# Kernel optimization log

Measured on AMD Instinct MI355X. Metric: run time of the kernel, lower is better.

The kernel has to match this reference:

```python
import jax, jax.numpy as jnp
import numpy as np

N = 100000      # nodes
E = 1_600_000   # edges
IN = 128        # in_channels
HID = 32        # hidden_channels (per head)
HEADS = 4
NC = 10         # num_classes
NEG_SLOPE = 0.2 # GATConv leaky relu slope
BN_EPS = 1e-5


def _gat_conv(x, src, dst, W, a_src, a_dst, bias, heads, out_ch, concat):
    # x: [N, F_in]; W: [F_in, heads*out_ch]; a_src/a_dst: [heads, out_ch]
    n = x.shape[0]
    h = (x @ W).reshape(n, heads, out_ch)                    # [N,H,C]
    al_src = jnp.sum(h * a_src, axis=-1)                     # [N,H]
    al_dst = jnp.sum(h * a_dst, axis=-1)                     # [N,H]
    e = jax.nn.leaky_relu(al_src[src] + al_dst[dst], NEG_SLOPE)  # [E,H]
    # segment softmax over destination node
    m = jax.ops.segment_max(e, dst, num_segments=n)          # [N,H]
    ex = jnp.exp(e - m[dst])
    s = jax.ops.segment_sum(ex, dst, num_segments=n)         # [N,H]
    alpha = ex / (s[dst] + 1e-16)                            # [E,H]
    out = jax.ops.segment_sum(h[src] * alpha[:, :, None], dst, num_segments=n)  # [N,H,C]
    if concat:
        out = out.reshape(n, heads * out_ch)
    else:
        out = out.mean(axis=1)
    return out + bias


def _bn(x, gamma, beta, mean, var):
    # eval-mode BatchNorm1d with running stats
    return (x - mean) * jax.lax.rsqrt(var + BN_EPS) * gamma + beta


def setup_inputs() -> dict:
    key = jax.random.key(0)
    ks = iter(jax.random.split(key, 40))
    d = {}
    d['x'] = jax.random.normal(next(ks), (N, IN), dtype=jnp.float32)
    d['edge_index'] = jax.random.randint(next(ks), (2, E), 0, N, dtype=jnp.int32)
    dims = [(IN, HID, HEADS), (HID * HEADS, HID, HEADS), (HID * HEADS, HID, 1)]
    for i, (fin, c, h) in enumerate(dims):
        d[f'W{i}'] = jax.random.normal(next(ks), (fin, h * c), dtype=jnp.float32) * (1.0 / np.sqrt(fin))
        d[f'as{i}'] = jax.random.normal(next(ks), (h, c), dtype=jnp.float32) * 0.1
        d[f'ad{i}'] = jax.random.normal(next(ks), (h, c), dtype=jnp.float32) * 0.1
        bdim = h * c if i < 2 else c
        d[f'b{i}'] = jnp.zeros((bdim,), dtype=jnp.float32)
        d[f'g{i}'] = jax.random.uniform(next(ks), (bdim,), dtype=jnp.float32, minval=0.5, maxval=1.5)
        d[f'bt{i}'] = jax.random.normal(next(ks), (bdim,), dtype=jnp.float32) * 0.1
        d[f'm{i}'] = jax.random.normal(next(ks), (bdim,), dtype=jnp.float32) * 0.1
        d[f'v{i}'] = jax.random.uniform(next(ks), (bdim,), dtype=jnp.float32, minval=0.5, maxval=1.5)
    d['Wc'] = jax.random.normal(next(ks), (HID, NC), dtype=jnp.float32) * (1.0 / np.sqrt(HID))
    d['bc'] = jnp.zeros((NC,), dtype=jnp.float32)
    return d


def reference(x, edge_index, W0, as0, ad0, b0, g0, bt0, m0, v0,
              W1, as1, ad1, b1, g1, bt1, m1, v1,
              W2, as2, ad2, b2, g2, bt2, m2, v2, Wc, bc):
    src, dst = edge_index[0], edge_index[1]
    # layer 0: concat heads
    h = _gat_conv(x, src, dst, W0, as0, ad0, b0, HEADS, HID, True)
    h = jax.nn.elu(_bn(h, g0, bt0, m0, v0))
    # layer 1: concat heads
    h = _gat_conv(h, src, dst, W1, as1, ad1, b1, HEADS, HID, True)
    h = jax.nn.elu(_bn(h, g1, bt1, m1, v1))
    # layer 2: single head, no concat
    h = _gat_conv(h, src, dst, W2, as2, ad2, b2, 1, HID, False)
    h = jax.nn.elu(_bn(h, g2, bt2, m2, v2))
    # dropout is identity in eval mode
    return h @ Wc + bc
```

## Files before the change

### kernel.cpp

```cpp
#include <hip/hip_runtime.h>
#include <hip/hip_bf16.h>
#include <math.h>

#define NN   100000
#define NE   1600000
#define FIN  128
#define HID  32
#define NHEADS 4
#define NCLS 10

typedef unsigned int uint32;
typedef __fp16 half2_t __attribute__((ext_vector_type(2)));
typedef __fp16 half8_t __attribute__((ext_vector_type(8)));
typedef float  f32x4   __attribute__((ext_vector_type(4)));

__device__ __forceinline__ uint32 packh2(float a, float b) {
    half2_t h = __builtin_amdgcn_cvt_pkrtz(a, b);
    return __builtin_bit_cast(uint32, h);
}
__device__ __forceinline__ float h_lo(uint32 v) {
    return (float)__builtin_bit_cast(half2_t, v)[0];
}
__device__ __forceinline__ float h_hi(uint32 v) {
    return (float)__builtin_bit_cast(half2_t, v)[1];
}
__device__ __forceinline__ half8_t as_h8(uint4 v) {
    return __builtin_bit_cast(half8_t, v);
}

__global__ void zero_i32(int* __restrict__ p, int n) {
    int i = blockIdx.x * blockDim.x + threadIdx.x;
    if (i < n) p[i] = 0;
}

__global__ void hist_rank_kernel(const int* __restrict__ dst, int* __restrict__ cnt,
                                 int* __restrict__ rank, int e) {
    const int t0 = blockIdx.x * (blockDim.x * 4) + threadIdx.x;
    int d[4];
    bool a[4];
#pragma unroll
    for (int k = 0; k < 4; ++k) {
        const int j = t0 + k * 256;
        a[k] = (j < e);
        d[k] = a[k] ? dst[j] : 0;
    }
    int r[4];
#pragma unroll
    for (int k = 0; k < 4; ++k)
        if (a[k]) r[k] = atomicAdd(&cnt[d[k]], 1);
#pragma unroll
    for (int k = 0; k < 4; ++k) {
        const int j = t0 + k * 256;
        if (a[k]) rank[j] = r[k];
    }
}

__global__ void scan_block_sums(const int* __restrict__ cnt, int* __restrict__ bsum, int n) {
    __shared__ int sm[256];
    int i = blockIdx.x * 256 + threadIdx.x;
    int v = (i < n) ? cnt[i] : 0;
    sm[threadIdx.x] = v;
    __syncthreads();
    for (int off = 128; off > 0; off >>= 1) {
        if (threadIdx.x < off) sm[threadIdx.x] += sm[threadIdx.x + off];
        __syncthreads();
    }
    if (threadIdx.x == 0) bsum[blockIdx.x] = sm[0];
}

__global__ void scan_single(const int* __restrict__ bsum, int* __restrict__ boff, int nb) {
    __shared__ int sm[512];
    int t = threadIdx.x;
    int v = (t < nb) ? bsum[t] : 0;
    sm[t] = v;
    __syncthreads();
    for (int off = 1; off < 512; off <<= 1) {
        int u = (t >= off) ? sm[t - off] : 0;
        __syncthreads();
        sm[t] += u;
        __syncthreads();
    }
    if (t < nb) boff[t] = sm[t] - v;
}

__global__ void scan_final(const int* __restrict__ cnt, const int* __restrict__ boff,
                           int* __restrict__ rowptr, int n) {
    __shared__ int sm[256];
    int i = blockIdx.x * 256 + threadIdx.x;
    int v = (i < n) ? cnt[i] : 0;
    sm[threadIdx.x] = v;
    __syncthreads();
    for (int off = 1; off < 256; off <<= 1) {
        int u = (threadIdx.x >= off) ? sm[threadIdx.x - off] : 0;
        __syncthreads();
        sm[threadIdx.x] += u;
        __syncthreads();
    }
    int incl = sm[threadIdx.x];
    int excl = incl - v;
    if (i < n) rowptr[i] = boff[blockIdx.x] + excl;
    if (i == n - 1) rowptr[n] = boff[blockIdx.x] + incl;
}

__global__ void scatter_kernel(const int* __restrict__ src, const int* __restrict__ dst,
                               const int* __restrict__ rank, const int* __restrict__ rowptr,
                               int* __restrict__ esrc, int e) {
    const int t0 = blockIdx.x * (blockDim.x * 4) + threadIdx.x;
#pragma unroll
    for (int k = 0; k < 4; ++k) {
        const int j = t0 + k * 256;
        if (j < e) {
            const int d = dst[j];
            esrc[rowptr[d] + rank[j]] = src[j];
        }
    }
}

__global__ void conv_x_kernel(const float* __restrict__ x, uint32* __restrict__ Xh, int n4) {
    int i = blockIdx.x * blockDim.x + threadIdx.x;
    if (i >= n4) return;
    const float4 v = ((const float4*)x)[i];
    ((uint2*)Xh)[i] = make_uint2(packh2(v.x, v.y), packh2(v.z, v.w));
}

__global__ void conv_w_kernel(const float* __restrict__ W0, const float* __restrict__ W1,
                              const float* __restrict__ W2, uint32* __restrict__ Wt0,
                              uint32* __restrict__ Wt1, uint32* __restrict__ Wt2) {
    int t = blockIdx.x * blockDim.x + threadIdx.x;
    if (t < 8192) {
        const int nn = t >> 6, ku = t & 63;
        Wt0[t] = packh2(W0[(2 * ku) * 128 + nn], W0[(2 * ku + 1) * 128 + nn]);
    } else if (t < 16384) {
        const int l = t - 8192;
        const int nn = l >> 6, ku = l & 63;
        Wt1[l] = packh2(W1[(2 * ku) * 128 + nn], W1[(2 * ku + 1) * 128 + nn]);
    } else if (t < 18432) {
        const int l = t - 16384;
        const int nn = l >> 6, ku = l & 63;
        Wt2[l] = packh2(W2[(2 * ku) * 32 + nn], W2[(2 * ku + 1) * 32 + nn]);
    }
}

template <int FOUT, int H>
__global__ __launch_bounds__(256) void gemm_mfma(const uint32* __restrict__ Xh,
                                                 const uint32* __restrict__ Wt,
                                                 const float* __restrict__ a_s,
                                                 const float* __restrict__ a_d,
                                                 float* __restrict__ alS,
                                                 float* __restrict__ alD,
                                                 uint32* __restrict__ Outh, int n) {
    constexpr int NT = FOUT / 16;
    const int wave = threadIdx.x >> 6;
    const int lane = threadIdx.x & 63;
    const int c = lane & 15;
    const int q = lane >> 4;
    const int row0 = blockIdx.x * 128 + wave * 32;

    int r0 = row0 + c;
    int r1 = row0 + 16 + c;
    if (r0 >= n) r0 = n - 1;
    if (r1 >= n) r1 = n - 1;

    f32x4 acc[2][NT];
#pragma unroll
    for (int m = 0; m < 2; ++m)
#pragma unroll
        for (int nt = 0; nt < NT; ++nt) acc[m][nt] = (f32x4){0.f, 0.f, 0.f, 0.f};

    const uint4* XU = (const uint4*)Xh;
    const uint4* WU = (const uint4*)Wt;

#pragma unroll
    for (int ks = 0; ks < 4; ++ks) {
        const half8_t a0 = as_h8(XU[(size_t)r0 * 16 + ks * 4 + q]);
        const half8_t a1 = as_h8(XU[(size_t)r1 * 16 + ks * 4 + q]);
#pragma unroll
        for (int nt = 0; nt < NT; ++nt) {
            const half8_t b = as_h8(WU[(nt * 16 + c) * 16 + ks * 4 + q]);
            acc[0][nt] = __builtin_amdgcn_mfma_f32_16x16x32_f16(a0, b, acc[0][nt], 0, 0, 0);
            acc[1][nt] = __builtin_amdgcn_mfma_f32_16x16x32_f16(a1, b, acc[1][nt], 0, 0, 0);
        }
    }

    float asv[NT], adv[NT];
#pragma unroll
    for (int nt = 0; nt < NT; ++nt) {
        asv[nt] = a_s[c + 16 * nt];
        adv[nt] = a_d[c + 16 * nt];
    }

#pragma unroll
    for (int m = 0; m < 2; ++m) {
#pragma unroll
        for (int reg = 0; reg < 4; ++reg) {
            const int grow = row0 + m * 16 + q * 4 + reg;
            const bool ok = (grow < n);
            if constexpr (H == 4) {
                float ps[4], pd[4];
#pragma unroll
                for (int h = 0; h < 4; ++h) {
                    ps[h] = acc[m][2 * h][reg] * asv[2 * h] + acc[m][2 * h + 1][reg] * asv[2 * h + 1];
                    pd[h] = acc[m][2 * h][reg] * adv[2 * h] + acc[m][2 * h + 1][reg] * adv[2 * h + 1];
                }
#pragma unroll
                for (int off = 1; off < 16; off <<= 1) {
#pragma unroll
                    for (int h = 0; h < 4; ++h) {
                        ps[h] += __shfl_xor(ps[h], off);
                        pd[h] += __shfl_xor(pd[h], off);
                    }
                }
                if (c < 4 && ok) {
                    const float vs = (c == 0) ? ps[0] : (c == 1) ? ps[1] : (c == 2) ? ps[2] : ps[3];
                    const float vd = (c == 0) ? pd[0] : (c == 1) ? pd[1] : (c == 2) ? pd[2] : pd[3];
                    alS[(size_t)grow * 4 + c] = vs;
                    alD[(size_t)grow * 4 + c] = vd;
                }
            } else {
                float ps = acc[m][0][reg] * asv[0] + acc[m][1][reg] * asv[1];
                float pd = acc[m][0][reg] * adv[0] + acc[m][1][reg] * adv[1];
#pragma unroll
                for (int off = 1; off < 16; off <<= 1) {
                    ps += __shfl_xor(ps, off);
                    pd += __shfl_xor(pd, off);
                }
                if (c == 0 && ok) {
                    alS[grow] = ps;
                    alD[grow] = pd;
                }
            }
#pragma unroll
            for (int nt = 0; nt < NT; ++nt) {
                const float v = acc[m][nt][reg];
                const float o = __shfl_xor(v, 1);
                if (((c & 1) == 0) && ok) {
                    Outh[(size_t)grow * (FOUT / 2) + nt * 8 + (c >> 1)] = packh2(v, o);
                }
            }
        }
    }
}

template <int H, int C>
__global__ __launch_bounds__(256) void gat_aggregate(
    const uint32* __restrict__ Hb,
    const int* __restrict__ rowptr, const int* __restrict__ esrc,
    const float* __restrict__ alS, const float* __restrict__ alD,
    const float* __restrict__ bias, const float* __restrict__ gamma,
    const float* __restrict__ beta, const float* __restrict__ bnmean,
    const float* __restrict__ bnvar, uint32* __restrict__ B16, int n) {
    constexpr int F  = H * C;
    constexpr int RW = F / 2;
    constexpr int NW = 4;
    __shared__ __align__(16) int   s_src[NW][68];
    __shared__ __align__(16) float s_ex[NW][H][68];

    const int wave = threadIdx.x >> 6;
    const int lane = threadIdx.x & 63;
    const int d    = blockIdx.x * NW + wave;
    if (d >= n) return;

    if (lane < 4) {
        s_src[wave][64 + lane] = 0;
#pragma unroll
        for (int h = 0; h < H; ++h) s_ex[wave][h][64 + lane] = 0.f;
    }
    __builtin_amdgcn_wave_barrier();

    const int beg = rowptr[d], end = rowptr[d + 1];
    float al_d[H], sl[H];
#pragma unroll
    for (int h = 0; h < H; ++h) {
        al_d[h] = alD[(size_t)d * H + h];
        sl[h]   = 0.f;
    }
    float acc0 = 0.f, acc1 = 0.f;
    const int head = (H == 4) ? (lane >> 4) : 0;

    for (int base = beg; base < end; base += 64) {
        const int j   = base + lane;
        const bool act = (j < end);
        int sj = 0;
        float ex[H];
        if (act) {
            sj = esrc[j];
            if constexpr (H == 4) {
                float4 av = *(const float4*)(alS + (size_t)sj * 4);
                float t0 = av.x + al_d[0], t1 = av.y + al_d[1];
                float t2 = av.z + al_d[2], t3 = av.w + al_d[3];
                t0 = t0 > 0.f ? t0 : 0.2f * t0;
                t1 = t1 > 0.f ? t1 : 0.2f * t1;
                t2 = t2 > 0.f ? t2 : 0.2f * t2;
                t3 = t3 > 0.f ? t3 : 0.2f * t3;
                ex[0] = __expf(t0); ex[1] = __expf(t1);
                ex[2] = __expf(t2); ex[3] = __expf(t3);
            } else {
                float t0 = alS[sj] + al_d[0];
                t0 = t0 > 0.f ? t0 : 0.2f * t0;
                ex[0] = __expf(t0);
            }
        } else {
#pragma unroll
            for (int h = 0; h < H; ++h) ex[h] = 0.f;
        }
#pragma unroll
        for (int h = 0; h < H; ++h) {
            s_ex[wave][h][lane] = ex[h];
            sl[h] += ex[h];
        }
        s_src[wave][lane] = sj;
        __builtin_amdgcn_wave_barrier();

        const int cc = min(64, end - base);
        if constexpr (H == 4) {
            const int ccr = (cc + 7) & ~7;
            for (int jj = 0; jj < ccr; jj += 8) {
                const int4   sa = *(const int4*)  &s_src[wave][jj];
                const int4   sb = *(const int4*)  &s_src[wave][jj + 4];
                const float4 wa = *(const float4*)&s_ex[wave][head][jj];
                const float4 wb = *(const float4*)&s_ex[wave][head][jj + 4];
                const int b0 = __builtin_amdgcn_readfirstlane(sa.x);
                const int b1 = __builtin_amdgcn_readfirstlane(sa.y);
                const int b2 = __builtin_amdgcn_readfirstlane(sa.z);
                const int b3 = __builtin_amdgcn_readfirstlane(sa.w);
                const int b4 = __builtin_amdgcn_readfirstlane(sb.x);
                const int b5 = __builtin_amdgcn_readfirstlane(sb.y);
                const int b6 = __builtin_amdgcn_readfirstlane(sb.z);
                const int b7 = __builtin_amdgcn_readfirstlane(sb.w);
                const uint32 v0 = Hb[(size_t)b0 * RW + lane];
                const uint32 v1 = Hb[(size_t)b1 * RW + lane];
                const uint32 v2 = Hb[(size_t)b2 * RW + lane];
                const uint32 v3 = Hb[(size_t)b3 * RW + lane];
                const uint32 v4 = Hb[(size_t)b4 * RW + lane];
                const uint32 v5 = Hb[(size_t)b5 * RW + lane];
                const uint32 v6 = Hb[(size_t)b6 * RW + lane];
                const uint32 v7 = Hb[(size_t)b7 * RW + lane];
                acc0 = fmaf(h_lo(v0), wa.x, acc0); acc1 = fmaf(h_hi(v0), wa.x, acc1);
                acc0 = fmaf(h_lo(v1), wa.y, acc0); acc1 = fmaf(h_hi(v1), wa.y, acc1);
                acc0 = fmaf(h_lo(v2), wa.z, acc0); acc1 = fmaf(h_hi(v2), wa.z, acc1);
                acc0 = fmaf(h_lo(v3), wa.w, acc0); acc1 = fmaf(h_hi(v3), wa.w, acc1);
                acc0 = fmaf(h_lo(v4), wb.x, acc0); acc1 = fmaf(h_hi(v4), wb.x, acc1);
                acc0 = fmaf(h_lo(v5), wb.y, acc0); acc1 = fmaf(h_hi(v5), wb.y, acc1);
                acc0 = fmaf(h_lo(v6), wb.z, acc0); acc1 = fmaf(h_hi(v6), wb.z, acc1);
                acc0 = fmaf(h_lo(v7), wb.w, acc0); acc1 = fmaf(h_hi(v7), wb.w, acc1);
            }
        } else {
            const int g  = lane >> 4;
            const int li = lane & 15;
            for (int jj = 0; jj < cc; jj += 4) {
                const int   idx = jj + g;
                const int   sj2 = s_src[wave][idx];
                const float w   = s_ex[wave][0][idx];
                const uint32 v  = Hb[(size_t)sj2 * RW + li];
                acc0 = fmaf(h_lo(v), w, acc0);
                acc1 = fmaf(h_hi(v), w, acc1);
            }
        }
        __builtin_amdgcn_wave_barrier();
    }

#pragma unroll
    for (int h = 0; h < H; ++h) {
#pragma unroll
        for (int off = 32; off > 0; off >>= 1) sl[h] += __shfl_xor(sl[h], off);
    }
    float sh;
    if constexpr (H == 4) {
        float a = (head & 1) ? sl[1] : sl[0];
        float b = (head & 1) ? sl[3] : sl[2];
        sh = (head & 2) ? b : a;
    } else {
        sh = sl[0];
        acc0 += __shfl_xor(acc0, 16); acc0 += __shfl_xor(acc0, 32);
        acc1 += __shfl_xor(acc1, 16); acc1 += __shfl_xor(acc1, 32);
    }

    const float inv = 1.f / (sh + 1e-16f);
    const int li  = (F == 128) ? lane : (lane & 15);
    const int c0 = 2 * li, c1 = 2 * li + 1;
    const bool wr = (F == 128) || (lane < 16);
    if (wr) {
        float o0 = acc0 * inv, o1 = acc1 * inv;
        float y0 = (o0 + bias[c0] - bnmean[c0]) * rsqrtf(bnvar[c0] + 1e-5f) * gamma[c0] + beta[c0];
        float y1 = (o1 + bias[c1] - bnmean[c1]) * rsqrtf(bnvar[c1] + 1e-5f) * gamma[c1] + beta[c1];
        y0 = y0 > 0.f ? y0 : expm1f(y0);
        y1 = y1 > 0.f ? y1 : expm1f(y1);
        B16[(size_t)d * RW + li] = packh2(y0, y1);
    }
}

__global__ void classifier_kernel(const uint32* __restrict__ H3, const float* __restrict__ Wc,
                                  const float* __restrict__ bc, float* __restrict__ out, int n) {
    int t  = blockIdx.x * blockDim.x + threadIdx.x;
    int ni = t / NCLS, c = t % NCLS;
    if (ni >= n) return;
    const uint32* row = H3 + (size_t)ni * 16;
    float a = bc[c];
#pragma unroll
    for (int u = 0; u < 16; ++u) {
        const uint32 v = row[u];
        a = fmaf(h_lo(v), Wc[(2 * u) * NCLS + c], a);
        a = fmaf(h_hi(v), Wc[(2 * u + 1) * NCLS + c], a);
    }
    out[(size_t)ni * NCLS + c] = a;
}

static inline char* align256(char* p) {
    return (char*)(((uintptr_t)p + 255) & ~(uintptr_t)255);
}

extern "C" void kernel_launch(void* const* d_in, const int* in_sizes, int n_in,
                              void* d_out, int out_size, void* d_ws, size_t ws_size,
                              hipStream_t stream) {
    const float* x  = (const float*)d_in[0];
    const int*   ei = (const int*)d_in[1];
    const int N = in_sizes[0] / FIN;
    const int E = in_sizes[1] / 2;
    const int* src = ei;
    const int* dst = ei + E;

    const float *W0 = (const float*)d_in[2],  *as0 = (const float*)d_in[3],
                *ad0 = (const float*)d_in[4], *b0 = (const float*)d_in[5],
                *g0 = (const float*)d_in[6],  *bt0 = (const float*)d_in[7],
                *m0 = (const float*)d_in[8],  *v0 = (const float*)d_in[9];
    const float *W1 = (const float*)d_in[10], *as1 = (const float*)d_in[11],
                *ad1 = (const float*)d_in[12],*b1 = (const float*)d_in[13],
                *g1 = (const float*)d_in[14], *bt1 = (const float*)d_in[15],
                *m1 = (const float*)d_in[16], *v1 = (const float*)d_in[17];
    const float *W2 = (const float*)d_in[18], *as2 = (const float*)d_in[19],
                *ad2 = (const float*)d_in[20],*b2 = (const float*)d_in[21],
                *g2 = (const float*)d_in[22], *bt2 = (const float*)d_in[23],
                *m2 = (const float*)d_in[24], *v2 = (const float*)d_in[25];
    const float *Wc = (const float*)d_in[26], *bc = (const float*)d_in[27];
    float* out = (float*)d_out;

    char* p = (char*)d_ws;
    uint32* Xh  = (uint32*)p;   p = align256(p + (size_t)N * 64 * 4);
    uint32* Ht  = (uint32*)p;   p = align256(p + (size_t)N * 64 * 4);
    uint32* B16 = (uint32*)p;   p = align256(p + (size_t)N * 64 * 4);
    uint32* Wt0 = (uint32*)p;   p = align256(p + 8192 * 4);
    uint32* Wt1 = (uint32*)p;   p = align256(p + 8192 * 4);
    uint32* Wt2 = (uint32*)p;   p = align256(p + 2048 * 4);
    float* alS = (float*)p;     p = align256(p + (size_t)N * NHEADS * 4);
    float* alD = (float*)p;     p = align256(p + (size_t)N * NHEADS * 4);
    int* cnt = (int*)p;         p = align256(p + (size_t)N * 4);
    int* rowptr = (int*)p;      p = align256(p + (size_t)(N + 1) * 4);
    int* rank = (int*)p;        p = align256(p + (size_t)E * 4);
    int* esrc = (int*)p;        p = align256(p + (size_t)E * 4);
    int* bsum = (int*)p;        p = align256(p + 512 * 4);
    int* boff = (int*)p;        p = align256(p + 512 * 4);
    (void)ws_size; (void)n_in; (void)out_size;

    const int NB = (N + 255) / 256;
    const int EB4 = (E + 1023) / 1024;

    zero_i32<<<NB, 256, 0, stream>>>(cnt, N);
    hist_rank_kernel<<<EB4, 256, 0, stream>>>(dst, cnt, rank, E);
    scan_block_sums<<<NB, 256, 0, stream>>>(cnt, bsum, N);
    scan_single<<<1, 512, 0, stream>>>(bsum, boff, NB);
    scan_final<<<NB, 256, 0, stream>>>(cnt, boff, rowptr, N);
    scatter_kernel<<<EB4, 256, 0, stream>>>(src, dst, rank, rowptr, esrc, E);

    conv_x_kernel<<<(N * 32 + 255) / 256, 256, 0, stream>>>(x, Xh, N * 32);
    conv_w_kernel<<<72, 256, 0, stream>>>(W0, W1, W2, Wt0, Wt1, Wt2);

    const int GB = (N + 127) / 128;
    const int AB = (N + 3) / 4;

    gemm_mfma<128, 4><<<GB, 256, 0, stream>>>(Xh, Wt0, as0, ad0, alS, alD, Ht, N);
    gat_aggregate<4, 32><<<AB, 256, 0, stream>>>(Ht, rowptr, esrc, alS, alD,
                                                 b0, g0, bt0, m0, v0, B16, N);
    gemm_mfma<128, 4><<<GB, 256, 0, stream>>>(B16, Wt1, as1, ad1, alS, alD, Ht, N);
    gat_aggregate<4, 32><<<AB, 256, 0, stream>>>(Ht, rowptr, esrc, alS, alD,
                                                 b1, g1, bt1, m1, v1, B16, N);
    gemm_mfma<32, 1><<<GB, 256, 0, stream>>>(B16, Wt2, as2, ad2, alS, alD, Ht, N);
    gat_aggregate<1, 32><<<AB, 256, 0, stream>>>(Ht, rowptr, esrc, alS, alD,
                                                 b2, g2, bt2, m2, v2, B16, N);
    classifier_kernel<<<(N * NCLS + 255) / 256, 256, 0, stream>>>(B16, Wc, bc, out, N);
}
```

Measured before the change: 546.0 us.

## Restructure GAT aggregation to per-lane uint4 gathers and fold BN constants

Measured after the change: 545.3 us. About the same (-0.1%).

```diff
diff --git a/kernel.cpp b/kernel.cpp
--- a/kernel.cpp
+++ b/kernel.cpp
@@ -141,6 +141,26 @@
     }
 }
 
+__global__ void bn_prep_kernel(
+    const float* __restrict__ b0, const float* __restrict__ g0, const float* __restrict__ bt0,
+    const float* __restrict__ m0, const float* __restrict__ v0,
+    const float* __restrict__ b1, const float* __restrict__ g1, const float* __restrict__ bt1,
+    const float* __restrict__ m1, const float* __restrict__ v1,
+    const float* __restrict__ b2, const float* __restrict__ g2, const float* __restrict__ bt2,
+    const float* __restrict__ m2, const float* __restrict__ v2,
+    float* __restrict__ A, float* __restrict__ B) {
+    const int t = threadIdx.x;
+    const float *b, *g, *bt, *m, *v;
+    int c;
+    if (t < 128)      { b = b0; g = g0; bt = bt0; m = m0; v = v0; c = t; }
+    else if (t < 256) { b = b1; g = g1; bt = bt1; m = m1; v = v1; c = t - 128; }
+    else if (t < 288) { b = b2; g = g2; bt = bt2; m = m2; v = v2; c = t - 256; }
+    else return;
+    const float s = g[c] * rsqrtf(v[c] + 1e-5f);
+    A[t] = s;
+    B[t] = bt[c] + (b[c] - m[c]) * s;
+}
+
 template <int FOUT, int H>
 __global__ __launch_bounds__(256) void gemm_mfma(const uint32* __restrict__ Xh,
                                                  const uint32* __restrict__ Wt,
@@ -246,146 +266,87 @@
     const uint32* __restrict__ Hb,
     const int* __restrict__ rowptr, const int* __restrict__ esrc,
     const float* __restrict__ alS, const float* __restrict__ alD,
-    const float* __restrict__ bias, const float* __restrict__ gamma,
-    const float* __restrict__ beta, const float* __restrict__ bnmean,
-    const float* __restrict__ bnvar, uint32* __restrict__ B16, int n) {
-    constexpr int F  = H * C;
-    constexpr int RW = F / 2;
-    constexpr int NW = 4;
-    __shared__ __align__(16) int   s_src[NW][68];
-    __shared__ __align__(16) float s_ex[NW][H][68];
+    const float* __restrict__ bnA, const float* __restrict__ bnB,
+    uint32* __restrict__ B16, int n) {
+    constexpr int F    = H * C;
+    constexpr int RU4  = F / 8;
+    constexpr int SLOTS = 64 / RU4;
+    constexpr int UNROLL = 16 / SLOTS;
 
     const int wave = threadIdx.x >> 6;
     const int lane = threadIdx.x & 63;
-    const int d    = blockIdx.x * NW + wave;
+    int d = blockIdx.x * 4 + wave;
     if (d >= n) return;
-
-    if (lane < 4) {
-        s_src[wave][64 + lane] = 0;
-#pragma unroll
-        for (int h = 0; h < H; ++h) s_ex[wave][h][64 + lane] = 0.f;
-    }
-    __builtin_amdgcn_wave_barrier();
-
-    const int beg = rowptr[d], end = rowptr[d + 1];
-    float al_d[H], sl[H];
-#pragma unroll
-    for (int h = 0; h < H; ++h) {
-        al_d[h] = alD[(size_t)d * H + h];
-        sl[h]   = 0.f;
-    }
-    float acc0 = 0.f, acc1 = 0.f;
-    const int head = (H == 4) ? (lane >> 4) : 0;
-
-    for (int base = beg; base < end; base += 64) {
-        const int j   = base + lane;
-        const bool act = (j < end);
-        int sj = 0;
-        float ex[H];
-        if (act) {
-            sj = esrc[j];
-            if constexpr (H == 4) {
-                float4 av = *(const float4*)(alS + (size_t)sj * 4);
-                float t0 = av.x + al_d[0], t1 = av.y + al_d[1];
-                float t2 = av.z + al_d[2], t3 = av.w + al_d[3];
-                t0 = t0 > 0.f ? t0 : 0.2f * t0;
-                t1 = t1 > 0.f ? t1 : 0.2f * t1;
-                t2 = t2 > 0.f ? t2 : 0.2f * t2;
-                t3 = t3 > 0.f ? t3 : 0.2f * t3;
-                ex[0] = __expf(t0); ex[1] = __expf(t1);
-                ex[2] = __expf(t2); ex[3] = __expf(t3);
-            } else {
-                float t0 = alS[sj] + al_d[0];
-                t0 = t0 > 0.f ? t0 : 0.2f * t0;
-                ex[0] = __expf(t0);
-            }
-        } else {
-#pragma unroll
-            for (int h = 0; h < H; ++h) ex[h] = 0.f;
+    d = __builtin_amdgcn_readfirstlane(d);
+
+    const int li = lane & (RU4 - 1);
+    const int g  = lane / RU4;
+    const int head = (H == 4) ? (li >> 2) : 0;
+
+    const float ald = alD[(size_t)d * H + head];
+    const int beg = rowptr[d];
+    const int end = rowptr[d + 1];
+    const int endm1 = end - 1;
+
+    float acc[8];
+#pragma unroll
+    for (int k = 0; k < 8; ++k) acc[k] = 0.f;
+    float den = 0.f;
+
+    const uint4* HbU4 = (const uint4*)Hb;
+
+    for (int base = beg; base < end; base += 16) {
+#pragma unroll
+        for (int u = 0; u < UNROLL; ++u) {
+            const int j  = base + u * SLOTS + g;
+            const bool act = (j < end);
+            const int jc = act ? j : endm1;
+            const int sj = esrc[jc];
+            const float aw = (H == 4) ? alS[(size_t)sj * 4 + head] : alS[sj];
+            float t = aw + ald;
+            t = fmaxf(t, 0.2f * t);
+            const float ex = act ? __expf(t) : 0.f;
+            den += ex;
+            const uint4 v = HbU4[(size_t)sj * RU4 + li];
+            acc[0] = fmaf(h_lo(v.x), ex, acc[0]);
+            acc[1] = fmaf(h_hi(v.x), ex, acc[1]);
+            acc[2] = fmaf(h_lo(v.y), ex, acc[2]);
+            acc[3] = fmaf(h_hi(v.y), ex, acc[3]);
+            acc[4] = fmaf(h_lo(v.z), ex, acc[4]);
+            acc[5] = fmaf(h_hi(v.z), ex, acc[5]);
+            acc[6] = fmaf(h_lo(v.w), ex, acc[6]);
+            acc[7] = fmaf(h_hi(v.w), ex, acc[7]);
         }
-#pragma unroll
-        for (int h = 0; h < H; ++h) {
-            s_ex[wave][h][lane] = ex[h];
-            sl[h] += ex[h];
+    }
+
+#pragma unroll
+    for (int off = RU4; off < 64; off <<= 1) {
+#pragma unroll
+        for (int k = 0; k < 8; ++k) acc[k] += __shfl_xor(acc[k], off);
+        den += __shfl_xor(den, off);
+    }
+
+    if (lane < RU4) {
+        const float inv = 1.f / (den + 1e-16f);
+        const int c0 = 8 * li;
+        const float4 A0 = *(const float4*)(bnA + c0);
+        const float4 A1 = *(const float4*)(bnA + c0 + 4);
+        const float4 B0 = *(const float4*)(bnB + c0);
+        const float4 B1 = *(const float4*)(bnB + c0 + 4);
+        const float As[8] = {A0.x, A0.y, A0.z, A0.w, A1.x, A1.y, A1.z, A1.w};
+        const float Bs[8] = {B0.x, B0.y, B0.z, B0.w, B1.x, B1.y, B1.z, B1.w};
+        float y[8];
+#pragma unroll
+        for (int k = 0; k < 8; ++k) {
+            const float yy = acc[k] * inv * As[k] + Bs[k];
+            y[k] = yy > 0.f ? yy : expm1f(yy);
         }
-        s_src[wave][lane] = sj;
-        __builtin_amdgcn_wave_barrier();
-
-        const int cc = min(64, end - base);
-        if constexpr (H == 4) {
-            const int ccr = (cc + 7) & ~7;
-            for (int jj = 0; jj < ccr; jj += 8) {
-                const int4   sa = *(const int4*)  &s_src[wave][jj];
-                const int4   sb = *(const int4*)  &s_src[wave][jj + 4];
-                const float4 wa = *(const float4*)&s_ex[wave][head][jj];
-                const float4 wb = *(const float4*)&s_ex[wave][head][jj + 4];
-                const int b0 = __builtin_amdgcn_readfirstlane(sa.x);
-                const int b1 = __builtin_amdgcn_readfirstlane(sa.y);
-                const int b2 = __builtin_amdgcn_readfirstlane(sa.z);
-                const int b3 = __builtin_amdgcn_readfirstlane(sa.w);
-                const int b4 = __builtin_amdgcn_readfirstlane(sb.x);
-                const int b5 = __builtin_amdgcn_readfirstlane(sb.y);
-                const int b6 = __builtin_amdgcn_readfirstlane(sb.z);
-                const int b7 = __builtin_amdgcn_readfirstlane(sb.w);
-                const uint32 v0 = Hb[(size_t)b0 * RW + lane];
-                const uint32 v1 = Hb[(size_t)b1 * RW + lane];
-                const uint32 v2 = Hb[(size_t)b2 * RW + lane];
-                const uint32 v3 = Hb[(size_t)b3 * RW + lane];
-                const uint32 v4 = Hb[(size_t)b4 * RW + lane];
-                const uint32 v5 = Hb[(size_t)b5 * RW + lane];
-                const uint32 v6 = Hb[(size_t)b6 * RW + lane];
-                const uint32 v7 = Hb[(size_t)b7 * RW + lane];
-                acc0 = fmaf(h_lo(v0), wa.x, acc0); acc1 = fmaf(h_hi(v0), wa.x, acc1);
-                acc0 = fmaf(h_lo(v1), wa.y, acc0); acc1 = fmaf(h_hi(v1), wa.y, acc1);
-                acc0 = fmaf(h_lo(v2), wa.z, acc0); acc1 = fmaf(h_hi(v2), wa.z, acc1);
-                acc0 = fmaf(h_lo(v3), wa.w, acc0); acc1 = fmaf(h_hi(v3), wa.w, acc1);
-                acc0 = fmaf(h_lo(v4), wb.x, acc0); acc1 = fmaf(h_hi(v4), wb.x, acc1);
-                acc0 = fmaf(h_lo(v5), wb.y, acc0); acc1 = fmaf(h_hi(v5), wb.y, acc1);
-                acc0 = fmaf(h_lo(v6), wb.z, acc0); acc1 = fmaf(h_hi(v6), wb.z, acc1);
-                acc0 = fmaf(h_lo(v7), wb.w, acc0); acc1 = fmaf(h_hi(v7), wb.w, acc1);
-            }
-        } else {
-            const int g  = lane >> 4;
-            const int li = lane & 15;
-            for (int jj = 0; jj < cc; jj += 4) {
-                const int   idx = jj + g;
-                const int   sj2 = s_src[wave][idx];
-                const float w   = s_ex[wave][0][idx];
-                const uint32 v  = Hb[(size_t)sj2 * RW + li];
-                acc0 = fmaf(h_lo(v), w, acc0);
-                acc1 = fmaf(h_hi(v), w, acc1);
-            }
-        }
-        __builtin_amdgcn_wave_barrier();
-    }
-
-#pragma unroll
-    for (int h = 0; h < H; ++h) {
-#pragma unroll
-        for (int off = 32; off > 0; off >>= 1) sl[h] += __shfl_xor(sl[h], off);
-    }
-    float sh;
-    if constexpr (H == 4) {
-        float a = (head & 1) ? sl[1] : sl[0];
-        float b = (head & 1) ? sl[3] : sl[2];
-        sh = (head & 2) ? b : a;
-    } else {
-        sh = sl[0];
-        acc0 += __shfl_xor(acc0, 16); acc0 += __shfl_xor(acc0, 32);
-        acc1 += __shfl_xor(acc1, 16); acc1 += __shfl_xor(acc1, 32);
-    }
-
-    const float inv = 1.f / (sh + 1e-16f);
-    const int li  = (F == 128) ? lane : (lane & 15);
-    const int c0 = 2 * li, c1 = 2 * li + 1;
-    const bool wr = (F == 128) || (lane < 16);
-    if (wr) {
-        float o0 = acc0 * inv, o1 = acc1 * inv;
-        float y0 = (o0 + bias[c0] - bnmean[c0]) * rsqrtf(bnvar[c0] + 1e-5f) * gamma[c0] + beta[c0];
-        float y1 = (o1 + bias[c1] - bnmean[c1]) * rsqrtf(bnvar[c1] + 1e-5f) * gamma[c1] + beta[c1];
-        y0 = y0 > 0.f ? y0 : expm1f(y0);
-        y1 = y1 > 0.f ? y1 : expm1f(y1);
-        B16[(size_t)d * RW + li] = packh2(y0, y1);
+        uint4 o;
+        o.x = packh2(y[0], y[1]);
+        o.y = packh2(y[2], y[3]);
+        o.z = packh2(y[4], y[5]);
+        o.w = packh2(y[6], y[7]);
+        ((uint4*)B16)[(size_t)d * RU4 + li] = o;
     }
 }
 
@@ -449,6 +410,8 @@
     int* esrc = (int*)p;        p = align256(p + (size_t)E * 4);
     int* bsum = (int*)p;        p = align256(p + 512 * 4);
     int* boff = (int*)p;        p = align256(p + 512 * 4);
+    float* bnA = (float*)p;     p = align256(p + 288 * 4);
+    float* bnB = (float*)p;     p = align256(p + 288 * 4);
     (void)ws_size; (void)n_in; (void)out_size;
 
     const int NB = (N + 255) / 256;
@@ -463,18 +426,21 @@
 
     conv_x_kernel<<<(N * 32 + 255) / 256, 256, 0, stream>>>(x, Xh, N * 32);
     conv_w_kernel<<<72, 256, 0, stream>>>(W0, W1, W2, Wt0, Wt1, Wt2);
+    bn_prep_kernel<<<1, 320, 0, stream>>>(b0, g0, bt0, m0, v0,
+                                          b1, g1, bt1, m1, v1,
+                                          b2, g2, bt2, m2, v2, bnA, bnB);
 
     const int GB = (N + 127) / 128;
     const int AB = (N + 3) / 4;
 
     gemm_mfma<128, 4><<<GB, 256, 0, stream>>>(Xh, Wt0, as0, ad0, alS, alD, Ht, N);
     gat_aggregate<4, 32><<<AB, 256, 0, stream>>>(Ht, rowptr, esrc, alS, alD,
-                                                 b0, g0, bt0, m0, v0, B16, N);
+                                                 bnA, bnB, B16, N);
     gemm_mfma<128, 4><<<GB, 256, 0, stream>>>(B16, Wt1, as1, ad1, alS, alD, Ht, N);
     gat_aggregate<4, 32><<<AB, 256, 0, stream>>>(Ht, rowptr, esrc, alS, alD,
-                                                 b1, g1, bt1, m1, v1, B16, N);
+                                                 bnA + 128, bnB + 128, B16, N);
     gemm_mfma<32, 1><<<GB, 256, 0, stream>>>(B16, Wt2, as2, ad2, alS, alD, Ht, N);
     gat_aggregate<1, 32><<<AB, 256, 0, stream>>>(Ht, rowptr, esrc, alS, alD,
-                                                 b2, g2, bt2, m2, v2, B16, N);
+                                                 bnA + 256, bnB + 256, B16, N);
     classifier_kernel<<<(N * NCLS + 255) / 256, 256, 0, stream>>>(B16, Wc, bc, out, N);
 }
```
